# Kernel tuning notes

Hardware: AMD Instinct MI355X
Metric: run time of the kernel (lower is better)

Reference implementation:

```python
import jax, jax.numpy as jnp
import numpy as np

NUM_HEADS = 16
HEAD_SIZE = 64
N_EMBD = 1024


def setup_inputs() -> dict:
    key = jax.random.key(0)
    ks = jax.random.split(key, 6)
    B, T, C = 2, 2048, N_EMBD
    scale = 0.02
    return {
        "x": jax.random.normal(ks[0], (B, T, C), dtype=jnp.float32),
        "Wq": jax.random.normal(ks[1], (C, NUM_HEADS * HEAD_SIZE), dtype=jnp.float32) * scale,
        "Wk": jax.random.normal(ks[2], (C, NUM_HEADS * HEAD_SIZE), dtype=jnp.float32) * scale,
        "Wv": jax.random.normal(ks[3], (C, NUM_HEADS * HEAD_SIZE), dtype=jnp.float32) * scale,
        "Wo": jax.random.normal(ks[4], (NUM_HEADS * HEAD_SIZE, C), dtype=jnp.float32) * scale,
        "bo": jnp.zeros((C,), dtype=jnp.float32),
    }


def reference(x, Wq, Wk, Wv, Wo, bo):
    B, T, C = x.shape
    H, D = NUM_HEADS, HEAD_SIZE
    # QKV projections (no bias), reshape to [B, H, T, D]
    q = (x @ Wq).reshape(B, T, H, D).transpose(0, 2, 1, 3)
    k = (x @ Wk).reshape(B, T, H, D).transpose(0, 2, 1, 3)
    v = (x @ Wv).reshape(B, T, H, D).transpose(0, 2, 1, 3)
    # scaled dot-product scores [B, H, T, T]
    scores = jnp.einsum("bhqd,bhkd->bhqk", q, k) / jnp.sqrt(jnp.float32(D))
    causal = jnp.tril(jnp.ones((T, T), dtype=bool))
    scores = jnp.where(causal, scores, -jnp.inf)
    weights = jax.nn.softmax(scores, axis=-1)  # dropout = identity (eval)
    out = jnp.einsum("bhqk,bhkd->bhqd", weights, v)
    out = out.transpose(0, 2, 1, 3).reshape(B, T, H * D)
    return out @ Wo + bo
```

## Files before the change

kernel.cpp:

```cpp
#include <hip/hip_runtime.h>

typedef __attribute__((ext_vector_type(8))) _Float16 f16x8;
typedef __attribute__((ext_vector_type(4))) _Float16 f16x4;
typedef __attribute__((ext_vector_type(2))) _Float16 f16x2;
typedef __attribute__((ext_vector_type(2))) __fp16   fp16x2_raw;
typedef __attribute__((ext_vector_type(4))) float    f32x4;

#define NUM_HEADS 16
#define HEAD_D 64
#define EMB 1024
#define SEQ 2048
#define BATCH 2
#define MTOT (BATCH * SEQ)

#define QALPHA 0.18033688011112042f

__device__ __forceinline__ f16x2 cvt_pk_f16(float lo, float hi)
{
    fp16x2_raw r = __builtin_amdgcn_cvt_pkrtz(lo, hi);
    return __builtin_bit_cast(f16x2, r);
}

#if defined(__has_builtin)
#if __has_builtin(__builtin_amdgcn_exp2f)
#define HAVE_EXP2 1
#endif
#endif
__device__ __forceinline__ float fast_exp2(float x)
{
#ifdef HAVE_EXP2
    return __builtin_amdgcn_exp2f(x);
#else
    return __expf(x * 0.6931471805599453f);
#endif
}

#if defined(__has_builtin)
#if __has_builtin(__builtin_amdgcn_global_load_lds)
#define HAVE_GLOAD_LDS 1
#endif
#endif

__device__ __forceinline__ void stage16(const void* g, void* ldsWaveBase, int lane)
{
#ifdef HAVE_GLOAD_LDS
    __builtin_amdgcn_global_load_lds(
        (const __attribute__((address_space(1))) void*)g,
        (__attribute__((address_space(3))) void*)ldsWaveBase, 16, 0, 0);
    (void)lane;
#else
    *(f16x8*)((char*)ldsWaveBase + lane * 16) = *(const f16x8*)g;
#endif
}

__global__ __launch_bounds__(256) void prep_all(
    const float* __restrict__ x,
    const float* __restrict__ Wq, const float* __restrict__ Wk,
    const float* __restrict__ Wv, const float* __restrict__ Wo,
    _Float16* __restrict__ xh, _Float16* __restrict__ Wt,
    _Float16* __restrict__ Wto)
{
    const int z = blockIdx.z;
    if (z == 4) {
        int base = ((blockIdx.y * 32 + blockIdx.x) * 256 + threadIdx.x) * 2;
        #pragma unroll
        for (int t = 0; t < 2; ++t) {
            int i = base + t;
            float4 a = ((const float4*)x)[i * 2];
            float4 b = ((const float4*)x)[i * 2 + 1];
            f16x8 o;
            o[0] = (_Float16)a.x; o[1] = (_Float16)a.y;
            o[2] = (_Float16)a.z; o[3] = (_Float16)a.w;
            o[4] = (_Float16)b.x; o[5] = (_Float16)b.y;
            o[6] = (_Float16)b.z; o[7] = (_Float16)b.w;
            ((f16x8*)xh)[i] = o;
        }
        return;
    }
    const float* W = z == 0 ? Wq : (z == 1 ? Wk : (z == 2 ? Wv : Wo));
    _Float16* D = (z == 3) ? Wto : (Wt + (size_t)z * EMB * EMB);
    __shared__ float tile[32][33];
    const int tx = threadIdx.x & 31, ty = threadIdx.x >> 5;
    const int n0 = blockIdx.x * 32, k0 = blockIdx.y * 32;
    #pragma unroll
    for (int j = 0; j < 4; ++j)
        tile[ty + j * 8][tx] = W[(size_t)(k0 + ty + j * 8) * EMB + n0 + tx];
    __syncthreads();
    #pragma unroll
    for (int j = 0; j < 4; ++j)
        D[(size_t)(n0 + ty + j * 8) * EMB + k0 + tx] =
            (_Float16)tile[tx][ty + j * 8];
}

__global__ __launch_bounds__(256) void gemm_qkv(
    const _Float16* __restrict__ A, const _Float16* __restrict__ Bt,
    _Float16* __restrict__ Qh, _Float16* __restrict__ Kh,
    _Float16* __restrict__ VhT)
{
    __shared__ __align__(16) _Float16 As[128 * 32];
    __shared__ __align__(16) _Float16 Bs[128 * 32];

    const int tid = threadIdx.x;
    const int w = tid >> 6, lane = tid & 63;
    const int l15 = lane & 15, g4 = lane >> 4;
    const int wm = w >> 1, wn = w & 1;

    const int wg = blockIdx.y * gridDim.x + blockIdx.x;
    const int t  = (wg & 7) * 96 + (wg >> 3);
    const int bx = t >> 5, by = t & 31;
    const int row0 = by * 128, col0 = bx * 128;

    f32x4 acc[4][4];
    #pragma unroll
    for (int mt = 0; mt < 4; ++mt)
        #pragma unroll
        for (int nt = 0; nt < 4; ++nt)
            acc[mt][nt] = (f32x4){0.f, 0.f, 0.f, 0.f};

    for (int k0 = 0; k0 < EMB; k0 += 32) {
        __syncthreads();
        #pragma unroll
        for (int i = 0; i < 2; ++i) {
            int c = (i << 8) + tid;
            int row = c >> 2, u = c & 3;
            stage16(&A[(size_t)(row0 + row) * EMB + k0 + (u << 3)],
                    (char*)As + (i << 12) + (w << 10), lane);
            stage16(&Bt[(size_t)(col0 + row) * EMB + k0 + (u << 3)],
                    (char*)Bs + (i << 12) + (w << 10), lane);
        }
        __syncthreads();

        f16x8 af[4], bf[4];
        #pragma unroll
        for (int mt = 0; mt < 4; ++mt)
            af[mt] = *(const f16x8*)((const char*)As +
                     ((wm << 6) + (mt << 4) + l15) * 64 + (g4 << 4));
        #pragma unroll
        for (int nt = 0; nt < 4; ++nt)
            bf[nt] = *(const f16x8*)((const char*)Bs +
                     ((wn << 6) + (nt << 4) + l15) * 64 + (g4 << 4));
        #pragma unroll
        for (int mt = 0; mt < 4; ++mt)
            #pragma unroll
            for (int nt = 0; nt < 4; ++nt)
                acc[mt][nt] = __builtin_amdgcn_mfma_f32_16x16x32_f16(
                    af[mt], bf[nt], acc[mt][nt], 0, 0, 0);
    }

    #pragma unroll
    for (int mt = 0; mt < 4; ++mt) {
        int m = row0 + (wm << 6) + (mt << 4) + (g4 << 2);
        #pragma unroll
        for (int nt = 0; nt < 4; ++nt) {
            int gcol = col0 + (wn << 6) + (nt << 4) + l15;
            int proj = gcol >> 10, pc = gcol & 1023;
            int h = pc >> 6, d = pc & 63;
            int b = m >> 11, tt = m & 2047;
            int bh = b * NUM_HEADS + h;
            if (proj == 2) {
                f16x4 v4;
                v4[0] = (_Float16)acc[mt][nt][0];
                v4[1] = (_Float16)acc[mt][nt][1];
                v4[2] = (_Float16)acc[mt][nt][2];
                v4[3] = (_Float16)acc[mt][nt][3];
                *(f16x4*)&VhT[((size_t)bh * HEAD_D + d) * SEQ + tt] = v4;
            } else {
                _Float16* dst = proj == 0 ? Qh : Kh;
                float alpha = proj == 0 ? QALPHA : 1.0f;
                #pragma unroll
                for (int r = 0; r < 4; ++r)
                    dst[((size_t)bh * SEQ + tt + r) * HEAD_D + d] =
                        (_Float16)(acc[mt][nt][r] * alpha);
            }
        }
    }
}

__global__ __launch_bounds__(256) void gemm_out(
    const _Float16* __restrict__ A, const _Float16* __restrict__ Bt,
    float* __restrict__ outf, const float* __restrict__ bias)
{
    __shared__ __align__(16) _Float16 As[128 * 32];
    __shared__ __align__(16) _Float16 Bs[64 * 32];

    const int tid = threadIdx.x;
    const int w = tid >> 6, lane = tid & 63;
    const int l15 = lane & 15, g4 = lane >> 4;
    const int wm = w >> 1, wn = w & 1;

    const int wg = blockIdx.y * gridDim.x + blockIdx.x;
    const int t  = (wg & 7) * 64 + (wg >> 3);
    const int bx = t >> 5, by = t & 31;
    const int row0 = by * 128, col0 = bx * 64;

    f32x4 acc[4][2];
    #pragma unroll
    for (int mt = 0; mt < 4; ++mt)
        #pragma unroll
        for (int nt = 0; nt < 2; ++nt)
            acc[mt][nt] = (f32x4){0.f, 0.f, 0.f, 0.f};

    for (int k0 = 0; k0 < EMB; k0 += 32) {
        __syncthreads();
        #pragma unroll
        for (int i = 0; i < 2; ++i) {
            int c = (i << 8) + tid;
            int row = c >> 2, u = c & 3;
            stage16(&A[(size_t)(row0 + row) * EMB + k0 + (u << 3)],
                    (char*)As + (i << 12) + (w << 10), lane);
        }
        {
            int row = tid >> 2, u = tid & 3;
            stage16(&Bt[(size_t)(col0 + row) * EMB + k0 + (u << 3)],
                    (char*)Bs + (w << 10), lane);
        }
        __syncthreads();

        f16x8 af[4], bf[2];
        #pragma unroll
        for (int mt = 0; mt < 4; ++mt)
            af[mt] = *(const f16x8*)((const char*)As +
                     ((wm << 6) + (mt << 4) + l15) * 64 + (g4 << 4));
        #pragma unroll
        for (int nt = 0; nt < 2; ++nt)
            bf[nt] = *(const f16x8*)((const char*)Bs +
                     ((wn << 5) + (nt << 4) + l15) * 64 + (g4 << 4));
        #pragma unroll
        for (int mt = 0; mt < 4; ++mt)
            #pragma unroll
            for (int nt = 0; nt < 2; ++nt)
                acc[mt][nt] = __builtin_amdgcn_mfma_f32_16x16x32_f16(
                    af[mt], bf[nt], acc[mt][nt], 0, 0, 0);
    }

    #pragma unroll
    for (int mt = 0; mt < 4; ++mt) {
        int m = row0 + (wm << 6) + (mt << 4) + (g4 << 2);
        #pragma unroll
        for (int nt = 0; nt < 2; ++nt) {
            int gcol = col0 + (wn << 5) + (nt << 4) + l15;
            float bz = bias[gcol];
            #pragma unroll
            for (int r = 0; r < 4; ++r)
                outf[(size_t)(m + r) * EMB + gcol] = acc[mt][nt][r] + bz;
        }
    }
}

__device__ __forceinline__ void stage_kv_tile(
    const _Float16* __restrict__ KhB, const _Float16* __restrict__ VtB,
    int kv0, char* __restrict__ KsBuf, char* __restrict__ VtBuf,
    int w, int lane)
{
    #pragma unroll
    for (int i = 0; i < 2; ++i) {
        int c = (i << 8) + (w << 6) + lane;
        int row = c >> 3, u = c & 7;
        int us = u ^ (row & 7);
        stage16(&KhB[(size_t)(kv0 + row) * HEAD_D + (us << 3)],
                KsBuf + (i << 12) + (w << 10), lane);
        stage16(&VtB[(size_t)row * SEQ + kv0 + (us << 3)],
                VtBuf + (i << 12) + (w << 10), lane);
    }
}

__device__ __forceinline__ void attn_tile(
    const char* __restrict__ KsC, const char* __restrict__ VtC,
    char* __restrict__ pwv,
    f16x8 qf0, f16x8 qf1, f32x4 (&acc)[4], float& m, float& l,
    bool diag, int qrel, int l15, int g)
{
    f32x4 st[4];
    #pragma unroll
    for (int nt = 0; nt < 4; ++nt) {
        int kvl = (nt << 4) + l15;
        f16x8 kf0 = *(const f16x8*)&KsC[kvl * 128 + (((g << 4)) ^ ((kvl & 7) << 4))];
        f16x8 kf1 = *(const f16x8*)&KsC[kvl * 128 + ((64 + (g << 4)) ^ ((kvl & 7) << 4))];
        f32x4 z = (f32x4){0.f, 0.f, 0.f, 0.f};
        z = __builtin_amdgcn_mfma_f32_16x16x32_f16(kf0, qf0, z, 0, 0, 0);
        z = __builtin_amdgcn_mfma_f32_16x16x32_f16(kf1, qf1, z, 0, 0, 0);
        st[nt] = z;
    }
    if (diag) {
        #pragma unroll
        for (int nt = 0; nt < 4; ++nt)
            #pragma unroll
            for (int r = 0; r < 4; ++r)
                if ((nt << 4) + (g << 2) + r > qrel) st[nt][r] = -1e30f;
    }

    float mx;
    {
        float a0 = fmaxf(fmaxf(st[0][0], st[0][1]), fmaxf(st[0][2], st[0][3]));
        float a1 = fmaxf(fmaxf(st[1][0], st[1][1]), fmaxf(st[1][2], st[1][3]));
        float a2 = fmaxf(fmaxf(st[2][0], st[2][1]), fmaxf(st[2][2], st[2][3]));
        float a3 = fmaxf(fmaxf(st[3][0], st[3][1]), fmaxf(st[3][2], st[3][3]));
        mx = fmaxf(fmaxf(a0, a1), fmaxf(a2, a3));
    }

    if (!__all(mx - m <= 8.0f)) {
        float mxr = fmaxf(mx, __shfl_xor(mx, 16));
        mxr = fmaxf(mxr, __shfl_xor(mxr, 32));
        float nm = fmaxf(m, mxr);
        float sc = fast_exp2(m - nm);
        m = nm;
        l *= sc;
        #pragma unroll
        for (int r = 0; r < 4; ++r) {
            float scr = __shfl(sc, (g << 2) + r);
            acc[0][r] *= scr; acc[1][r] *= scr;
            acc[2][r] *= scr; acc[3][r] *= scr;
        }
    }

    float ps = 0.f;
    #pragma unroll
    for (int nt = 0; nt < 4; ++nt)
        #pragma unroll
        for (int r = 0; r < 4; ++r) {
            float p = fast_exp2(st[nt][r] - m);
            st[nt][r] = p;
            ps += p;
        }
    l += ps;

    #pragma unroll
    for (int nt = 0; nt < 4; ++nt)
        #pragma unroll
        for (int rr = 0; rr < 2; ++rr) {
            int kvb = (nt << 4) + (g << 2) + (rr << 1);
            f16x2 pv = cvt_pk_f16(st[nt][rr * 2], st[nt][rr * 2 + 1]);
            *(f16x2*)&pwv[l15 * 128 + ((kvb << 1) ^ ((l15 & 7) << 4))] = pv;
        }
    f16x8 pa0 = *(const f16x8*)&pwv[l15 * 128 + (((g << 4)) ^ ((l15 & 7) << 4))];
    f16x8 pa1 = *(const f16x8*)&pwv[l15 * 128 + ((64 + (g << 4)) ^ ((l15 & 7) << 4))];

    #pragma unroll
    for (int dn = 0; dn < 4; ++dn) {
        int d = (dn << 4) + l15;
        f16x8 vf0 = *(const f16x8*)&VtC[d * 128 + (((g << 4)) ^ ((d & 7) << 4))];
        f16x8 vf1 = *(const f16x8*)&VtC[d * 128 + ((64 + (g << 4)) ^ ((d & 7) << 4))];
        acc[dn] = __builtin_amdgcn_mfma_f32_16x16x32_f16(pa0, vf0, acc[dn], 0, 0, 0);
        acc[dn] = __builtin_amdgcn_mfma_f32_16x16x32_f16(pa1, vf1, acc[dn], 0, 0, 0);
    }
}

__device__ __forceinline__ void attn_tile2(
    const char* __restrict__ Ks0, const char* __restrict__ Vt0,
    const char* __restrict__ Ks1, const char* __restrict__ Vt1,
    char* __restrict__ pwv0, char* __restrict__ pwv1,
    f16x8 qf0, f16x8 qf1, f32x4 (&acc)[4], float& m, float& l,
    bool diag1, int qrel, int l15, int g)
{
    f32x4 st[8];
    #pragma unroll
    for (int nt = 0; nt < 4; ++nt) {
        int kvl = (nt << 4) + l15;
        int off0 = kvl * 128 + (((g << 4)) ^ ((kvl & 7) << 4));
        int off1 = kvl * 128 + ((64 + (g << 4)) ^ ((kvl & 7) << 4));
        f16x8 ka0 = *(const f16x8*)&Ks0[off0];
        f16x8 ka1 = *(const f16x8*)&Ks0[off1];
        f32x4 z = (f32x4){0.f, 0.f, 0.f, 0.f};
        z = __builtin_amdgcn_mfma_f32_16x16x32_f16(ka0, qf0, z, 0, 0, 0);
        z = __builtin_amdgcn_mfma_f32_16x16x32_f16(ka1, qf1, z, 0, 0, 0);
        st[nt] = z;
        f16x8 kb0 = *(const f16x8*)&Ks1[off0];
        f16x8 kb1 = *(const f16x8*)&Ks1[off1];
        f32x4 z2 = (f32x4){0.f, 0.f, 0.f, 0.f};
        z2 = __builtin_amdgcn_mfma_f32_16x16x32_f16(kb0, qf0, z2, 0, 0, 0);
        z2 = __builtin_amdgcn_mfma_f32_16x16x32_f16(kb1, qf1, z2, 0, 0, 0);
        st[4 + nt] = z2;
    }
    if (diag1) {
        #pragma unroll
        for (int nt = 0; nt < 4; ++nt)
            #pragma unroll
            for (int r = 0; r < 4; ++r)
                if ((nt << 4) + (g << 2) + r > qrel) st[4 + nt][r] = -1e30f;
    }

    float mx;
    {
        float a = -1e30f;
        #pragma unroll
        for (int i = 0; i < 8; ++i)
            a = fmaxf(a, fmaxf(fmaxf(st[i][0], st[i][1]),
                               fmaxf(st[i][2], st[i][3])));
        mx = a;
    }

    if (!__all(mx - m <= 8.0f)) {
        float mxr = fmaxf(mx, __shfl_xor(mx, 16));
        mxr = fmaxf(mxr, __shfl_xor(mxr, 32));
        float nm = fmaxf(m, mxr);
        float sc = fast_exp2(m - nm);
        m = nm;
        l *= sc;
        #pragma unroll
        for (int r = 0; r < 4; ++r) {
            float scr = __shfl(sc, (g << 2) + r);
            acc[0][r] *= scr; acc[1][r] *= scr;
            acc[2][r] *= scr; acc[3][r] *= scr;
        }
    }

    float ps = 0.f;
    #pragma unroll
    for (int i = 0; i < 8; ++i)
        #pragma unroll
        for (int r = 0; r < 4; ++r) {
            float p = fast_exp2(st[i][r] - m);
            st[i][r] = p;
            ps += p;
        }
    l += ps;

    #pragma unroll
    for (int tile = 0; tile < 2; ++tile) {
        const f32x4* s4 = &st[tile << 2];
        const char* Vt = tile ? Vt1 : Vt0;
        char* pwv = tile ? pwv1 : pwv0;
        #pragma unroll
        for (int nt = 0; nt < 4; ++nt)
            #pragma unroll
            for (int rr = 0; rr < 2; ++rr) {
                int kvb = (nt << 4) + (g << 2) + (rr << 1);
                f16x2 pv = cvt_pk_f16(s4[nt][rr * 2], s4[nt][rr * 2 + 1]);
                *(f16x2*)&pwv[l15 * 128 + ((kvb << 1) ^ ((l15 & 7) << 4))] = pv;
            }
        f16x8 pa0 = *(const f16x8*)&pwv[l15 * 128 + (((g << 4)) ^ ((l15 & 7) << 4))];
        f16x8 pa1 = *(const f16x8*)&pwv[l15 * 128 + ((64 + (g << 4)) ^ ((l15 & 7) << 4))];
        #pragma unroll
        for (int dn = 0; dn < 4; ++dn) {
            int d = (dn << 4) + l15;
            f16x8 vf0 = *(const f16x8*)&Vt[d * 128 + (((g << 4)) ^ ((d & 7) << 4))];
            f16x8 vf1 = *(const f16x8*)&Vt[d * 128 + ((64 + (g << 4)) ^ ((d & 7) << 4))];
            acc[dn] = __builtin_amdgcn_mfma_f32_16x16x32_f16(pa0, vf0, acc[dn], 0, 0, 0);
            acc[dn] = __builtin_amdgcn_mfma_f32_16x16x32_f16(pa1, vf1, acc[dn], 0, 0, 0);
        }
    }
}

__global__ __launch_bounds__(256, 4) void attn_mfma(
    const _Float16* __restrict__ Qh, const _Float16* __restrict__ Kh,
    const _Float16* __restrict__ VhT, _Float16* __restrict__ O)
{
    __shared__ char lds[80 * 1024];
#define KSLOT(s) (lds + ((s) << 13))
#define VSLOT(s) (lds + 32768 + ((s) << 13))

    const int wg  = blockIdx.y * gridDim.x + blockIdx.x;
    const int idx = wg >> 3;
    const int bh  = (wg & 7) * 4 + (idx >> 4);
    const int qtA = idx & 15;
    const int qtB = (SEQ / 64 - 1) - qtA;
    const int q0A = qtA << 6, q0B = qtB << 6;
    const int tid = threadIdx.x;
    const int w = tid >> 6, lane = tid & 63;
    const int l15 = lane & 15, g = lane >> 4;

    const _Float16* KhB = Kh  + (size_t)bh * SEQ * HEAD_D;
    const _Float16* VtB = VhT + (size_t)bh * HEAD_D * SEQ;
    const size_t headbase = (size_t)bh * SEQ * HEAD_D;

    const int qrowA = q0A + (w << 4) + l15;
    const int qrowB = q0B + (w << 4) + l15;
    f16x8 qfA0 = *(const f16x8*)&Qh[headbase + (size_t)qrowA * HEAD_D + (g << 3)];
    f16x8 qfA1 = *(const f16x8*)&Qh[headbase + (size_t)qrowA * HEAD_D + 32 + (g << 3)];
    f16x8 qfB0 = *(const f16x8*)&Qh[headbase + (size_t)qrowB * HEAD_D + (g << 3)];
    f16x8 qfB1 = *(const f16x8*)&Qh[headbase + (size_t)qrowB * HEAD_D + 32 + (g << 3)];

    f32x4 accA[4], accB[4];
    #pragma unroll
    for (int dn = 0; dn < 4; ++dn) {
        accA[dn] = (f32x4){0.f, 0.f, 0.f, 0.f};
        accB[dn] = (f32x4){0.f, 0.f, 0.f, 0.f};
    }
    float mA = -1e30f, lA = 0.f, mB = -1e30f, lB = 0.f;

    stage_kv_tile(KhB, VtB, 0,  KSLOT(0), VSLOT(0), w, lane);
    stage_kv_tile(KhB, VtB, 64, KSLOT(1), VSLOT(1), w, lane);
    __syncthreads();

    char* pwvA = lds + 65536 + (w << 11);
    char* pwvB = lds + 73728 + (w << 11);
    const int qrel = (w << 4) + l15;

    for (int kt = 0; kt <= qtA; ++kt) {
        int pf = kt + 2;
        if (pf <= qtB)
            stage_kv_tile(KhB, VtB, pf << 6, KSLOT(pf & 3), VSLOT(pf & 3), w, lane);
        attn_tile(KSLOT(kt & 3), VSLOT(kt & 3), pwvA, qfA0, qfA1, accA, mA, lA,
                  kt == qtA, qrel, l15, g);
        attn_tile(KSLOT(kt & 3), VSLOT(kt & 3), pwvB, qfB0, qfB1, accB, mB, lB,
                  false, qrel, l15, g);
        __syncthreads();
    }

    {
        int kt = qtA + 1;
        int pf = kt + 2;
        if (pf <= qtB)
            stage_kv_tile(KhB, VtB, pf << 6, KSLOT(pf & 3), VSLOT(pf & 3), w, lane);
        attn_tile(KSLOT(kt & 3), VSLOT(kt & 3), pwvB, qfB0, qfB1, accB, mB, lB,
                  kt == qtB, qrel, l15, g);
        __syncthreads();
    }

    for (int kt = qtA + 2; kt < qtB; kt += 2) {
        int pf0 = kt + 2, pf1 = kt + 3;
        if (pf0 <= qtB)
            stage_kv_tile(KhB, VtB, pf0 << 6, KSLOT(pf0 & 3), VSLOT(pf0 & 3), w, lane);
        if (pf1 <= qtB)
            stage_kv_tile(KhB, VtB, pf1 << 6, KSLOT(pf1 & 3), VSLOT(pf1 & 3), w, lane);
        attn_tile2(KSLOT(kt & 3), VSLOT(kt & 3),
                   KSLOT((kt + 1) & 3), VSLOT((kt + 1) & 3),
                   pwvB, pwvA, qfB0, qfB1, accB, mB, lB,
                   (kt + 1) == qtB, qrel, l15, g);
        __syncthreads();
    }

    lA += __shfl_xor(lA, 16); lA += __shfl_xor(lA, 32);
    lB += __shfl_xor(lB, 16); lB += __shfl_xor(lB, 32);
    const int b = bh >> 4, h = bh & 15;
    const float rlA = 1.f / lA, rlB = 1.f / lB;
    #pragma unroll
    for (int r = 0; r < 4; ++r) {
        float invA = __shfl(rlA, (g << 2) + r);
        float invB = __shfl(rlB, (g << 2) + r);
        int tokA = (b << 11) + q0A + (w << 4) + (g << 2) + r;
        int tokB = (b << 11) + q0B + (w << 4) + (g << 2) + r;
        #pragma unroll
        for (int dn = 0; dn < 4; ++dn) {
            O[(size_t)tokA * EMB + (h << 6) + (dn << 4) + l15] =
                (_Float16)(accA[dn][r] * invA);
            O[(size_t)tokB * EMB + (h << 6) + (dn << 4) + l15] =
                (_Float16)(accB[dn][r] * invB);
        }
    }
#undef KSLOT
#undef VSLOT
}

extern "C" void kernel_launch(void* const* d_in, const int* in_sizes, int n_in,
                              void* d_out, int out_size, void* d_ws, size_t ws_size,
                              hipStream_t stream)
{
    const float* x  = (const float*)d_in[0];
    const float* Wq = (const float*)d_in[1];
    const float* Wk = (const float*)d_in[2];
    const float* Wv = (const float*)d_in[3];
    const float* Wo = (const float*)d_in[4];
    const float* bo = (const float*)d_in[5];
    float* out = (float*)d_out;

    const size_t ME = (size_t)MTOT * EMB;
    const size_t WE = (size_t)EMB * EMB;
    const size_t need = (5 * ME + 4 * WE) * sizeof(_Float16);
    if (ws_size < need) return;

    _Float16* xh  = (_Float16*)d_ws;
    _Float16* Wt  = xh + ME;
    _Float16* Wto = Wt + 3 * WE;
    _Float16* Qh  = Wto + WE;
    _Float16* Kh  = Qh + ME;
    _Float16* VhT = Kh + ME;
    _Float16* Ow  = VhT + ME;

    prep_all<<<dim3(EMB / 32, EMB / 32, 5), 256, 0, stream>>>(
        x, Wq, Wk, Wv, Wo, xh, Wt, Wto);

    gemm_qkv<<<dim3(3 * EMB / 128, MTOT / 128), 256, 0, stream>>>(
        xh, Wt, Qh, Kh, VhT);

    attn_mfma<<<dim3(SEQ / 128, BATCH * NUM_HEADS), 256, 0, stream>>>(Qh, Kh, VhT, Ow);

    gemm_out<<<dim3(EMB / 64, MTOT / 128), 256, 0, stream>>>(
        Ow, Wto, out, bo);
}
```

Baseline: 111.2 us.

## Fuse dual query-block processing with shared K/V fragments and two-tile steps

In the shared-prefix phase the kernel now processes both query blocks (A and B) in one routine that loads each K and V fragment from LDS once and feeds it to MFMAs for both blocks. It also advances two KV tiles per iteration with one barrier per pair, matching the later phase. This is meant to halve LDS fragment reads and barrier count in the first loop and expose more independent MFMAs. The cost is higher register pressure (two score sets of up to 8 tiles each), which under launch_bounds(256,4) could cause spills.

```diff
diff --git a/kernel.cpp b/kernel.cpp
--- a/kernel.cpp
+++ b/kernel.cpp
@@ -264,6 +264,58 @@
     }
 }
 
+template <int NT>
+__device__ __forceinline__ void softmax_update(
+    f32x4 (&s)[NT], f32x4 (&acc)[4], float& m, float& l, int g)
+{
+    float mx = -1e30f;
+    #pragma unroll
+    for (int i = 0; i < NT; ++i)
+        mx = fmaxf(mx, fmaxf(fmaxf(s[i][0], s[i][1]), fmaxf(s[i][2], s[i][3])));
+
+    if (!__all(mx - m <= 8.0f)) {
+        float mxr = fmaxf(mx, __shfl_xor(mx, 16));
+        mxr = fmaxf(mxr, __shfl_xor(mxr, 32));
+        float nm = fmaxf(m, mxr);
+        float sc = fast_exp2(m - nm);
+        m = nm;
+        l *= sc;
+        #pragma unroll
+        for (int r = 0; r < 4; ++r) {
+            float scr = __shfl(sc, (g << 2) + r);
+            acc[0][r] *= scr; acc[1][r] *= scr;
+            acc[2][r] *= scr; acc[3][r] *= scr;
+        }
+    }
+
+    float ps = 0.f;
+    #pragma unroll
+    for (int i = 0; i < NT; ++i)
+        #pragma unroll
+        for (int r = 0; r < 4; ++r) {
+            float p = fast_exp2(s[i][r] - m);
+            s[i][r] = p;
+            ps += p;
+        }
+    l += ps;
+}
+
+__device__ __forceinline__ void p_roundtrip(
+    const f32x4* s4, char* __restrict__ pwv, int l15, int g,
+    f16x8& pa0, f16x8& pa1)
+{
+    #pragma unroll
+    for (int nt = 0; nt < 4; ++nt)
+        #pragma unroll
+        for (int rr = 0; rr < 2; ++rr) {
+            int kvb = (nt << 4) + (g << 2) + (rr << 1);
+            f16x2 pv = cvt_pk_f16(s4[nt][rr * 2], s4[nt][rr * 2 + 1]);
+            *(f16x2*)&pwv[l15 * 128 + ((kvb << 1) ^ ((l15 & 7) << 4))] = pv;
+        }
+    pa0 = *(const f16x8*)&pwv[l15 * 128 + (((g << 4)) ^ ((l15 & 7) << 4))];
+    pa1 = *(const f16x8*)&pwv[l15 * 128 + ((64 + (g << 4)) ^ ((l15 & 7) << 4))];
+}
+
 __device__ __forceinline__ void attn_tile(
     const char* __restrict__ KsC, const char* __restrict__ VtC,
     char* __restrict__ pwv,
@@ -289,51 +341,10 @@
                 if ((nt << 4) + (g << 2) + r > qrel) st[nt][r] = -1e30f;
     }
 
-    float mx;
-    {
-        float a0 = fmaxf(fmaxf(st[0][0], st[0][1]), fmaxf(st[0][2], st[0][3]));
-        float a1 = fmaxf(fmaxf(st[1][0], st[1][1]), fmaxf(st[1][2], st[1][3]));
-        float a2 = fmaxf(fmaxf(st[2][0], st[2][1]), fmaxf(st[2][2], st[2][3]));
-        float a3 = fmaxf(fmaxf(st[3][0], st[3][1]), fmaxf(st[3][2], st[3][3]));
-        mx = fmaxf(fmaxf(a0, a1), fmaxf(a2, a3));
-    }
-
-    if (!__all(mx - m <= 8.0f)) {
-        float mxr = fmaxf(mx, __shfl_xor(mx, 16));
-        mxr = fmaxf(mxr, __shfl_xor(mxr, 32));
-        float nm = fmaxf(m, mxr);
-        float sc = fast_exp2(m - nm);
-        m = nm;
-        l *= sc;
-        #pragma unroll
-        for (int r = 0; r < 4; ++r) {
-            float scr = __shfl(sc, (g << 2) + r);
-            acc[0][r] *= scr; acc[1][r] *= scr;
-            acc[2][r] *= scr; acc[3][r] *= scr;
-        }
-    }
-
-    float ps = 0.f;
-    #pragma unroll
-    for (int nt = 0; nt < 4; ++nt)
-        #pragma unroll
-        for (int r = 0; r < 4; ++r) {
-            float p = fast_exp2(st[nt][r] - m);
-            st[nt][r] = p;
-            ps += p;
-        }
-    l += ps;
-
-    #pragma unroll
-    for (int nt = 0; nt < 4; ++nt)
-        #pragma unroll
-        for (int rr = 0; rr < 2; ++rr) {
-            int kvb = (nt << 4) + (g << 2) + (rr << 1);
-            f16x2 pv = cvt_pk_f16(st[nt][rr * 2], st[nt][rr * 2 + 1]);
-            *(f16x2*)&pwv[l15 * 128 + ((kvb << 1) ^ ((l15 & 7) << 4))] = pv;
-        }
-    f16x8 pa0 = *(const f16x8*)&pwv[l15 * 128 + (((g << 4)) ^ ((l15 & 7) << 4))];
-    f16x8 pa1 = *(const f16x8*)&pwv[l15 * 128 + ((64 + (g << 4)) ^ ((l15 & 7) << 4))];
+    softmax_update<4>(st, acc, m, l, g);
+
+    f16x8 pa0, pa1;
+    p_roundtrip(st, pwv, l15, g, pa0, pa1);
 
     #pragma unroll
     for (int dn = 0; dn < 4; ++dn) {
@@ -342,6 +353,126 @@
         f16x8 vf1 = *(const f16x8*)&VtC[d * 128 + ((64 + (g << 4)) ^ ((d & 7) << 4))];
         acc[dn] = __builtin_amdgcn_mfma_f32_16x16x32_f16(pa0, vf0, acc[dn], 0, 0, 0);
         acc[dn] = __builtin_amdgcn_mfma_f32_16x16x32_f16(pa1, vf1, acc[dn], 0, 0, 0);
+    }
+}
+
+__device__ __forceinline__ void attn_tile_dual(
+    const char* __restrict__ KsC, const char* __restrict__ VtC,
+    char* __restrict__ pwvA, char* __restrict__ pwvB,
+    f16x8 qfA0, f16x8 qfA1, f16x8 qfB0, f16x8 qfB1,
+    f32x4 (&accA)[4], f32x4 (&accB)[4],
+    float& mA, float& lA, float& mB, float& lB,
+    bool diagA, int qrel, int l15, int g)
+{
+    f32x4 sA[4], sB[4];
+    #pragma unroll
+    for (int nt = 0; nt < 4; ++nt) {
+        int kvl = (nt << 4) + l15;
+        f16x8 kf0 = *(const f16x8*)&KsC[kvl * 128 + (((g << 4)) ^ ((kvl & 7) << 4))];
+        f16x8 kf1 = *(const f16x8*)&KsC[kvl * 128 + ((64 + (g << 4)) ^ ((kvl & 7) << 4))];
+        f32x4 zA = (f32x4){0.f, 0.f, 0.f, 0.f};
+        zA = __builtin_amdgcn_mfma_f32_16x16x32_f16(kf0, qfA0, zA, 0, 0, 0);
+        zA = __builtin_amdgcn_mfma_f32_16x16x32_f16(kf1, qfA1, zA, 0, 0, 0);
+        sA[nt] = zA;
+        f32x4 zB = (f32x4){0.f, 0.f, 0.f, 0.f};
+        zB = __builtin_amdgcn_mfma_f32_16x16x32_f16(kf0, qfB0, zB, 0, 0, 0);
+        zB = __builtin_amdgcn_mfma_f32_16x16x32_f16(kf1, qfB1, zB, 0, 0, 0);
+        sB[nt] = zB;
+    }
+    if (diagA) {
+        #pragma unroll
+        for (int nt = 0; nt < 4; ++nt)
+            #pragma unroll
+            for (int r = 0; r < 4; ++r)
+                if ((nt << 4) + (g << 2) + r > qrel) sA[nt][r] = -1e30f;
+    }
+
+    softmax_update<4>(sA, accA, mA, lA, g);
+    softmax_update<4>(sB, accB, mB, lB, g);
+
+    f16x8 paA0, paA1, paB0, paB1;
+    p_roundtrip(sA, pwvA, l15, g, paA0, paA1);
+    p_roundtrip(sB, pwvB, l15, g, paB0, paB1);
+
+    #pragma unroll
+    for (int dn = 0; dn < 4; ++dn) {
+        int d = (dn << 4) + l15;
+        f16x8 vf0 = *(const f16x8*)&VtC[d * 128 + (((g << 4)) ^ ((d & 7) << 4))];
+        f16x8 vf1 = *(const f16x8*)&VtC[d * 128 + ((64 + (g << 4)) ^ ((d & 7) << 4))];
+        accA[dn] = __builtin_amdgcn_mfma_f32_16x16x32_f16(paA0, vf0, accA[dn], 0, 0, 0);
+        accA[dn] = __builtin_amdgcn_mfma_f32_16x16x32_f16(paA1, vf1, accA[dn], 0, 0, 0);
+        accB[dn] = __builtin_amdgcn_mfma_f32_16x16x32_f16(paB0, vf0, accB[dn], 0, 0, 0);
+        accB[dn] = __builtin_amdgcn_mfma_f32_16x16x32_f16(paB1, vf1, accB[dn], 0, 0, 0);
+    }
+}
+
+__device__ __forceinline__ void attn_tile2_dual(
+    const char* __restrict__ Ks0, const char* __restrict__ Vt0,
+    const char* __restrict__ Ks1, const char* __restrict__ Vt1,
+    char* __restrict__ pwvA, char* __restrict__ pwvB,
+    f16x8 qfA0, f16x8 qfA1, f16x8 qfB0, f16x8 qfB1,
+    f32x4 (&accA)[4], f32x4 (&accB)[4],
+    float& mA, float& lA, float& mB, float& lB,
+    bool diagA1, int qrel, int l15, int g)
+{
+    f32x4 sA[8], sB[8];
+    #pragma unroll
+    for (int nt = 0; nt < 4; ++nt) {
+        int kvl = (nt << 4) + l15;
+        int off0 = kvl * 128 + (((g << 4)) ^ ((kvl & 7) << 4));
+        int off1 = kvl * 128 + ((64 + (g << 4)) ^ ((kvl & 7) << 4));
+        {
+            f16x8 kf0 = *(const f16x8*)&Ks0[off0];
+            f16x8 kf1 = *(const f16x8*)&Ks0[off1];
+            f32x4 zA = (f32x4){0.f, 0.f, 0.f, 0.f};
+            zA = __builtin_amdgcn_mfma_f32_16x16x32_f16(kf0, qfA0, zA, 0, 0, 0);
+            zA = __builtin_amdgcn_mfma_f32_16x16x32_f16(kf1, qfA1, zA, 0, 0, 0);
+            sA[nt] = zA;
+            f32x4 zB = (f32x4){0.f, 0.f, 0.f, 0.f};
+            zB = __builtin_amdgcn_mfma_f32_16x16x32_f16(kf0, qfB0, zB, 0, 0, 0);
+            zB = __builtin_amdgcn_mfma_f32_16x16x32_f16(kf1, qfB1, zB, 0, 0, 0);
+            sB[nt] = zB;
+        }
+        {
+            f16x8 kf0 = *(const f16x8*)&Ks1[off0];
+            f16x8 kf1 = *(const f16x8*)&Ks1[off1];
+            f32x4 zA = (f32x4){0.f, 0.f, 0.f, 0.f};
+            zA = __builtin_amdgcn_mfma_f32_16x16x32_f16(kf0, qfA0, zA, 0, 0, 0);
+            zA = __builtin_amdgcn_mfma_f32_16x16x32_f16(kf1, qfA1, zA, 0, 0, 0);
+            sA[4 + nt] = zA;
+            f32x4 zB = (f32x4){0.f, 0.f, 0.f, 0.f};
+            zB = __builtin_amdgcn_mfma_f32_16x16x32_f16(kf0, qfB0, zB, 0, 0, 0);
+            zB = __builtin_amdgcn_mfma_f32_16x16x32_f16(kf1, qfB1, zB, 0, 0, 0);
+            sB[4 + nt] = zB;
+        }
+    }
+    if (diagA1) {
+        #pragma unroll
+        for (int nt = 0; nt < 4; ++nt)
+            #pragma unroll
+            for (int r = 0; r < 4; ++r)
+                if ((nt << 4) + (g << 2) + r > qrel) sA[4 + nt][r] = -1e30f;
+    }
+
+    softmax_update<8>(sA, accA, mA, lA, g);
+    softmax_update<8>(sB, accB, mB, lB, g);
+
+    #pragma unroll
+    for (int tile = 0; tile < 2; ++tile) {
+        const char* Vt = tile ? Vt1 : Vt0;
+        f16x8 paA0, paA1, paB0, paB1;
+        p_roundtrip(&sA[tile << 2], pwvA, l15, g, paA0, paA1);
+        p_roundtrip(&sB[tile << 2], pwvB, l15, g, paB0, paB1);
+        #pragma unroll
+        for (int dn = 0; dn < 4; ++dn) {
+            int d = (dn << 4) + l15;
+            f16x8 vf0 = *(const f16x8*)&Vt[d * 128 + (((g << 4)) ^ ((d & 7) << 4))];
+            f16x8 vf1 = *(const f16x8*)&Vt[d * 128 + ((64 + (g << 4)) ^ ((d & 7) << 4))];
+            accA[dn] = __builtin_amdgcn_mfma_f32_16x16x32_f16(paA0, vf0, accA[dn], 0, 0, 0);
+            accA[dn] = __builtin_amdgcn_mfma_f32_16x16x32_f16(paA1, vf1, accA[dn], 0, 0, 0);
+            accB[dn] = __builtin_amdgcn_mfma_f32_16x16x32_f16(paB0, vf0, accB[dn], 0, 0, 0);
+            accB[dn] = __builtin_amdgcn_mfma_f32_16x16x32_f16(paB1, vf1, accB[dn], 0, 0, 0);
+        }
     }
 }
 
@@ -379,57 +510,14 @@
                 if ((nt << 4) + (g << 2) + r > qrel) st[4 + nt][r] = -1e30f;
     }
 
-    float mx;
-    {
-        float a = -1e30f;
-        #pragma unroll
-        for (int i = 0; i < 8; ++i)
-            a = fmaxf(a, fmaxf(fmaxf(st[i][0], st[i][1]),
-                               fmaxf(st[i][2], st[i][3])));
-        mx = a;
-    }
-
-    if (!__all(mx - m <= 8.0f)) {
-        float mxr = fmaxf(mx, __shfl_xor(mx, 16));
-        mxr = fmaxf(mxr, __shfl_xor(mxr, 32));
-        float nm = fmaxf(m, mxr);
-        float sc = fast_exp2(m - nm);
-        m = nm;
-        l *= sc;
-        #pragma unroll
-        for (int r = 0; r < 4; ++r) {
-            float scr = __shfl(sc, (g << 2) + r);
-            acc[0][r] *= scr; acc[1][r] *= scr;
-            acc[2][r] *= scr; acc[3][r] *= scr;
-        }
-    }
-
-    float ps = 0.f;
-    #pragma unroll
-    for (int i = 0; i < 8; ++i)
-        #pragma unroll
-        for (int r = 0; r < 4; ++r) {
-            float p = fast_exp2(st[i][r] - m);
-            st[i][r] = p;
-            ps += p;
-        }
-    l += ps;
+    softmax_update<8>(st, acc, m, l, g);
 
     #pragma unroll
     for (int tile = 0; tile < 2; ++tile) {
-        const f32x4* s4 = &st[tile << 2];
         const char* Vt = tile ? Vt1 : Vt0;
         char* pwv = tile ? pwv1 : pwv0;
-        #pragma unroll
-        for (int nt = 0; nt < 4; ++nt)
-            #pragma unroll
-            for (int rr = 0; rr < 2; ++rr) {
-                int kvb = (nt << 4) + (g << 2) + (rr << 1);
-                f16x2 pv = cvt_pk_f16(s4[nt][rr * 2], s4[nt][rr * 2 + 1]);
-                *(f16x2*)&pwv[l15 * 128 + ((kvb << 1) ^ ((l15 & 7) << 4))] = pv;
-            }
-        f16x8 pa0 = *(const f16x8*)&pwv[l15 * 128 + (((g << 4)) ^ ((l15 & 7) << 4))];
-        f16x8 pa1 = *(const f16x8*)&pwv[l15 * 128 + ((64 + (g << 4)) ^ ((l15 & 7) << 4))];
+        f16x8 pa0, pa1;
+        p_roundtrip(&st[tile << 2], pwv, l15, g, pa0, pa1);
         #pragma unroll
         for (int dn = 0; dn < 4; ++dn) {
             int d = (dn << 4) + l15;
@@ -486,28 +574,42 @@
     char* pwvB = lds + 73728 + (w << 11);
     const int qrel = (w << 4) + l15;
 
-    for (int kt = 0; kt <= qtA; ++kt) {
+    int kt = 0;
+    for (; kt + 1 <= qtA; kt += 2) {
+        int pf0 = kt + 2, pf1 = kt + 3;
+        if (pf0 <= qtB)
+            stage_kv_tile(KhB, VtB, pf0 << 6, KSLOT(pf0 & 3), VSLOT(pf0 & 3), w, lane);
+        if (pf1 <= qtB)
+            stage_kv_tile(KhB, VtB, pf1 << 6, KSLOT(pf1 & 3), VSLOT(pf1 & 3), w, lane);
+        attn_tile2_dual(KSLOT(kt & 3), VSLOT(kt & 3),
+                        KSLOT((kt + 1) & 3), VSLOT((kt + 1) & 3),
+                        pwvA, pwvB, qfA0, qfA1, qfB0, qfB1,
+                        accA, accB, mA, lA, mB, lB,
+                        (kt + 1) == qtA, qrel, l15, g);
+        __syncthreads();
+    }
+    if (kt == qtA) {
         int pf = kt + 2;
         if (pf <= qtB)
             stage_kv_tile(KhB, VtB, pf << 6, KSLOT(pf & 3), VSLOT(pf & 3), w, lane);
-        attn_tile(KSLOT(kt & 3), VSLOT(kt & 3), pwvA, qfA0, qfA1, accA, mA, lA,
-                  kt == qtA, qrel, l15, g);
-        attn_tile(KSLOT(kt & 3), VSLOT(kt & 3), pwvB, qfB0, qfB1, accB, mB, lB,
-                  false, qrel, l15, g);
-        __syncthreads();
+        attn_tile_dual(KSLOT(kt & 3), VSLOT(kt & 3), pwvA, pwvB,
+                       qfA0, qfA1, qfB0, qfB1, accA, accB,
+                       mA, lA, mB, lB, true, qrel, l15, g);
+        __syncthreads();
+        ++kt;
     }
 
     {
-        int kt = qtA + 1;
         int pf = kt + 2;
         if (pf <= qtB)
             stage_kv_tile(KhB, VtB, pf << 6, KSLOT(pf & 3), VSLOT(pf & 3), w, lane);
         attn_tile(KSLOT(kt & 3), VSLOT(kt & 3), pwvB, qfB0, qfB1, accB, mB, lB,
                   kt == qtB, qrel, l15, g);
         __syncthreads();
-    }
-
-    for (int kt = qtA + 2; kt < qtB; kt += 2) {
+        ++kt;
+    }
+
+    for (; kt < qtB; kt += 2) {
         int pf0 = kt + 2, pf1 = kt + 3;
         if (pf0 <= qtB)
             stage_kv_tile(KhB, VtB, pf0 << 6, KSLOT(pf0 & 3), VSLOT(pf0 & 3), w, lane);
```

New measurement: 122.1 us. 1.1x slower.
